# Kernel optimization log

Hardware: AMD Instinct MI355X
Metric: run time of the kernel (lower is better)

The kernel has to match this reference:

```python
import jax, jax.numpy as jnp
import numpy as np

N_WIRES = 4
N_LAYERS = 2
DIM = 2 ** N_WIRES  # 16
EPS = 1e-5

# PennyLane convention: wire 0 is the most-significant bit of the basis index.
def _bit(i, w):
    return (i >> (N_WIRES - 1 - w)) & 1

# CNOT(control=w, target=(w+1)%N_WIRES) as a basis-state permutation on [DIM]
def _cnot_perm(c, t):
    perm = np.arange(DIM)
    for i in range(DIM):
        if _bit(i, c) == 1:
            perm[i] = i ^ (1 << (N_WIRES - 1 - t))
    return jnp.asarray(perm)

CNOT_PERMS = [_cnot_perm(w, (w + 1) % N_WIRES) for w in range(N_WIRES)]

# PauliZ expectation signs: +1 if bit w of basis state is 0 else -1, shape [N_WIRES, DIM]
SIGNS = jnp.asarray(np.array([[1.0 - 2.0 * _bit(i, w) for i in range(DIM)]
                              for w in range(N_WIRES)], dtype=np.float32))

def _rx(t):
    c = jnp.cos(t / 2).astype(jnp.complex64)
    s = (-1j * jnp.sin(t / 2)).astype(jnp.complex64)
    return jnp.stack([jnp.stack([c, s], -1), jnp.stack([s, c], -1)], -2)

def _ry(t):
    c = jnp.cos(t / 2).astype(jnp.complex64)
    s = jnp.sin(t / 2).astype(jnp.complex64)
    return jnp.stack([jnp.stack([c, -s], -1), jnp.stack([s, c], -1)], -2)

def _rz(t):
    e0 = jnp.exp(-1j * t.astype(jnp.complex64) / 2)
    e1 = jnp.exp(1j * t.astype(jnp.complex64) / 2)
    z = jnp.zeros_like(e0)
    return jnp.stack([jnp.stack([e0, z], -1), jnp.stack([z, e1], -1)], -2)

def _apply1q(state, U, w):
    # state: [B, DIM] complex64; U: [2,2] (shared) or [B,2,2] (per-sample)
    B = state.shape[0]
    st = state.reshape(B, 2 ** w, 2, 2 ** (N_WIRES - 1 - w))
    if U.ndim == 3:
        st = jnp.einsum('blkr,bjk->bljr', st, U)
    else:
        st = jnp.einsum('blkr,jk->bljr', st, U)
    return st.reshape(B, DIM)

def _circuit(angles, weights):
    # angles: [B, N_WIRES] float32, weights: [N_LAYERS, N_WIRES, 3]
    B = angles.shape[0]
    state = jnp.zeros((B, DIM), jnp.complex64).at[:, 0].set(1.0)
    # AngleEmbedding: RX(angle) per wire (per-sample angles)
    for w in range(N_WIRES):
        state = _apply1q(state, _rx(angles[:, w]), w)
    for l in range(N_LAYERS):
        for w in range(N_WIRES):
            state = _apply1q(state, _rx(weights[l, w, 0]), w)
            state = _apply1q(state, _ry(weights[l, w, 1]), w)
            state = _apply1q(state, _rz(weights[l, w, 2]), w)
        for w in range(N_WIRES):
            state = state[:, CNOT_PERMS[w]]
    probs = state.real ** 2 + state.imag ** 2  # [B, DIM]
    return probs @ SIGNS.T  # [B, N_WIRES]

def setup_inputs() -> dict:
    key = jax.random.key(0)
    k1, k2 = jax.random.split(key)
    B = 131072
    x = jax.random.normal(k1, (B, 1, 12, 12), dtype=jnp.float32)
    weights = jax.random.normal(k2, (N_LAYERS, N_WIRES, 3), dtype=jnp.float32)
    gamma = jnp.ones((N_WIRES,), jnp.float32)
    beta = jnp.zeros((N_WIRES,), jnp.float32)
    return {"x": x, "weights": weights, "gamma": gamma, "beta": beta}

def reference(x, weights, gamma, beta):
    B = x.shape[0]
    # avg_pool2d(kernel=6, stride=6) on [B,1,12,12] -> [B,1,2,2] -> [B,4]
    pooled = x.reshape(B, 1, 2, 6, 2, 6).mean(axis=(3, 5)).reshape(B, N_WIRES)
    q = _circuit(pooled, weights)  # [B, 4]
    # dropout p=0 is identity; BatchNorm1d (training mode: batch stats, biased var)
    mean = q.mean(axis=0)
    var = q.var(axis=0)
    return (q - mean) / jnp.sqrt(var + EPS) * gamma + beta
```

## Files before the change

### kernel.cpp

```cpp
#include <hip/hip_runtime.h>

#define WS_SUMS   352
#define N_REP     8

__global__ void k_pre(const float* __restrict__ W, float* __restrict__ ws){
  __shared__ float Ur[16][16];
  __shared__ float Uim[16][16];
  __shared__ float Mr[4][16][16];
  __shared__ float Mi[4][16][16];
  const int t = threadIdx.x;

  if (t < N_REP*8) ws[WS_SUMS + t] = 0.f;

  if (t < 16){
    float re[16], im[16];
    #pragma unroll
    for (int i = 0; i < 16; i++){ re[i] = 0.f; im[i] = 0.f; }
    re[t] = 1.f;

    #pragma unroll
    for (int l = 0; l < 2; l++){
      #pragma unroll
      for (int w = 0; w < 4; w++){
        const int m = 8 >> w;
        const float* g = W + (l*4 + w)*3;
        {
          float th = 0.5f*g[0], c = cosf(th), s = sinf(th);
          #pragma unroll
          for (int i0 = 0; i0 < 16; i0++) if (!(i0 & m)){
            int i1 = i0 | m;
            float a0r=re[i0], a0i=im[i0], a1r=re[i1], a1i=im[i1];
            re[i0] = c*a0r + s*a1i;  im[i0] = c*a0i - s*a1r;
            re[i1] = c*a1r + s*a0i;  im[i1] = c*a1i - s*a0r;
          }
        }
        {
          float th = 0.5f*g[1], c = cosf(th), s = sinf(th);
          #pragma unroll
          for (int i0 = 0; i0 < 16; i0++) if (!(i0 & m)){
            int i1 = i0 | m;
            float a0r=re[i0], a0i=im[i0], a1r=re[i1], a1i=im[i1];
            re[i0] = c*a0r - s*a1r;  im[i0] = c*a0i - s*a1i;
            re[i1] = s*a0r + c*a1r;  im[i1] = s*a0i + c*a1i;
          }
        }
        {
          float th = 0.5f*g[2], c = cosf(th), s = sinf(th);
          #pragma unroll
          for (int i0 = 0; i0 < 16; i0++) if (!(i0 & m)){
            int i1 = i0 | m;
            float a0r=re[i0], a0i=im[i0], a1r=re[i1], a1i=im[i1];
            re[i0] = c*a0r + s*a0i;  im[i0] = c*a0i - s*a0r;
            re[i1] = c*a1r - s*a1i;  im[i1] = c*a1i + s*a1r;
          }
        }
      }
      #pragma unroll
      for (int w = 0; w < 4; w++){
        const int mc = 8 >> w, mt = 8 >> ((w+1)&3);
        float nr[16], ni[16];
        #pragma unroll
        for (int i = 0; i < 16; i++){
          int src = (i & mc) ? (i ^ mt) : i;
          nr[i] = re[src]; ni[i] = im[src];
        }
        #pragma unroll
        for (int i = 0; i < 16; i++){ re[i] = nr[i]; im[i] = ni[i]; }
      }
    }
    #pragma unroll
    for (int k = 0; k < 16; k++){ Ur[k][t] = re[k]; Uim[k][t] = im[k]; }
  }
  __syncthreads();

  {
    const int j = t >> 4, i = t & 15;
    #pragma unroll
    for (int w = 0; w < 4; w++){
      const int zm = 8 >> w;
      float mr = 0.f, mi = 0.f;
      #pragma unroll
      for (int k = 0; k < 16; k++){
        float z = (k & zm) ? -1.f : 1.f;
        float ar = Ur[k][j], ai = Uim[k][j];
        float br = Ur[k][i], bi = Uim[k][i];
        mr += z*(ar*br + ai*bi);
        mi += z*(ar*bi - ai*br);
      }
      Mr[w][j][i] = mr;  Mi[w][j][i] = mi;
    }
  }
  __syncthreads();

  if (t < 81){
    int d0 = t/27, rem = t - d0*27;
    int d1 = rem/9;  rem -= d1*9;
    int d2 = rem/3,  d3 = rem - d2*3;
    int maskY = 0, maskZ = 0, mY = 0;
    if (d0 == 1){ maskY |= 8; mY++; } else if (d0 == 2) maskZ |= 8;
    if (d1 == 1){ maskY |= 4; mY++; } else if (d1 == 2) maskZ |= 4;
    if (d2 == 1){ maskY |= 2; mY++; } else if (d2 == 2) maskZ |= 2;
    if (d3 == 1){ maskY |= 1; mY++; } else if (d3 == 2) maskZ |= 1;
    const int mall = maskY | maskZ;
    const int sel  = mY & 3;
    #pragma unroll
    for (int w = 0; w < 4; w++){
      float c = 0.f;
      for (int i = 0; i < 16; i++){
        int j = i ^ maskY;
        float s = (__popc(i & mall) & 1) ? -1.f : 1.f;
        float val = (sel == 0) ?  Mr[w][j][i]
                  : (sel == 1) ?  Mi[w][j][i]
                  : (sel == 2) ? -Mr[w][j][i]
                  :              -Mi[w][j][i];
        c += s * val;
      }
      ws[t*4 + w] = c * 0.0625f;
    }
  }
}

__global__ __launch_bounds__(256) void k_main(const float* __restrict__ x,
                                              const float* __restrict__ C,
                                              float* __restrict__ qout,
                                              float* __restrict__ sums){
  __shared__ float wred[4][8];
  const int t = threadIdx.x;
  const size_t row = (size_t)blockIdx.x*256 + t;
  const float4* rp = (const float4*)(x + row*144);

  float aTL = 0.f, aTR = 0.f, aBL = 0.f, aBR = 0.f;
  #pragma unroll
  for (int ph = 0; ph < 3; ph++){
    float4 buf[12];
    #pragma unroll
    for (int j = 0; j < 12; j++) buf[j] = rp[ph*12 + j];
    #pragma unroll
    for (int j = 0; j < 12; j++){
      const int p  = ph*12 + j;
      const int cg = p % 3;
      float s01 = buf[j].x + buf[j].y, s23 = buf[j].z + buf[j].w;
      float L = (cg == 0) ? (s01 + s23) : ((cg == 1) ? s01 : 0.f);
      float R = (cg == 2) ? (s01 + s23) : ((cg == 1) ? s23 : 0.f);
      if (p < 18){ aTL += L; aTR += R; } else { aBL += L; aBR += R; }
    }
  }

  const float inv = 1.f/36.f;
  float s0,c0,s1,c1,s2,c2,s3,c3;
  __sincosf(aTL*inv, &s0, &c0);
  __sincosf(aTR*inv, &s1, &c1);
  __sincosf(aBL*inv, &s2, &c2);
  __sincosf(aBR*inv, &s3, &c3);
  const float g0[3] = {1.f, -s0, c0};
  const float g1[3] = {1.f, -s1, c1};
  const float g2[3] = {1.f, -s2, c2};
  const float g3[3] = {1.f, -s3, c3};

  float G01[9], G23[9];
  #pragma unroll
  for (int a = 0; a < 3; a++)
    #pragma unroll
    for (int b = 0; b < 3; b++){
      G01[a*3+b] = g0[a]*g1[b];
      G23[a*3+b] = g2[a]*g3[b];
    }

  float q0=0.f, q1=0.f, q2=0.f, q3=0.f;
  #pragma unroll
  for (int m = 0; m < 9; m++){
    #pragma unroll
    for (int l = 0; l < 9; l++){
      const int n = m*9 + l;
      float g = G01[m]*G23[l];
      q0 = fmaf(C[n*4+0], g, q0);
      q1 = fmaf(C[n*4+1], g, q1);
      q2 = fmaf(C[n*4+2], g, q2);
      q3 = fmaf(C[n*4+3], g, q3);
    }
  }

  ((float4*)qout)[row] = make_float4(q0, q1, q2, q3);

  float red[8] = {q0, q1, q2, q3, q0*q0, q1*q1, q2*q2, q3*q3};
  #pragma unroll
  for (int off = 32; off >= 1; off >>= 1){
    #pragma unroll
    for (int k = 0; k < 8; k++) red[k] += __shfl_down(red[k], off, 64);
  }
  const int lane = t & 63, wv = t >> 6;
  if (lane == 0){
    #pragma unroll
    for (int k = 0; k < 8; k++) wred[wv][k] = red[k];
  }
  __syncthreads();
  if (t < 8){
    float s = wred[0][t] + wred[1][t] + wred[2][t] + wred[3][t];
    atomicAdd(&sums[(blockIdx.x & (N_REP-1))*8 + t], s);
  }
}

__global__ __launch_bounds__(256) void k_statsnorm(float* __restrict__ out,
                                                   const float* __restrict__ sums,
                                                   const float* __restrict__ gamma,
                                                   const float* __restrict__ beta,
                                                   float invB){
  const int idx = blockIdx.x*256 + threadIdx.x;
  float sc[4], sh[4];
  #pragma unroll
  for (int w = 0; w < 4; w++){
    float s1 = 0.f, s2 = 0.f;
    #pragma unroll
    for (int rep = 0; rep < N_REP; rep++){
      s1 += sums[rep*8 + w];
      s2 += sums[rep*8 + 4 + w];
    }
    float mean  = s1 * invB;
    float var   = s2 * invB - mean*mean;
    float scale = gamma[w] * rsqrtf(var + 1e-5f);
    sc[w] = scale;
    sh[w] = fmaf(-mean, scale, beta[w]);
  }
  float4* o4 = (float4*)out;
  float4 qv = o4[idx];
  qv.x = fmaf(qv.x, sc[0], sh[0]);
  qv.y = fmaf(qv.y, sc[1], sh[1]);
  qv.z = fmaf(qv.z, sc[2], sh[2]);
  qv.w = fmaf(qv.w, sc[3], sh[3]);
  o4[idx] = qv;
}

extern "C" void kernel_launch(void* const* d_in, const int* in_sizes, int n_in,
                              void* d_out, int out_size, void* d_ws, size_t ws_size,
                              hipStream_t stream){
  const float* x     = (const float*)d_in[0];
  const float* W     = (const float*)d_in[1];
  const float* gamma = (const float*)d_in[2];
  const float* beta  = (const float*)d_in[3];
  float* ws  = (float*)d_ws;
  float* out = (float*)d_out;
  const int B = in_sizes[0] / 144;

  k_pre<<<1, 256, 0, stream>>>(W, ws);
  k_main<<<B/256, 256, 0, stream>>>(x, ws, out, ws + WS_SUMS);
  k_statsnorm<<<B/256, 256, 0, stream>>>(out, ws + WS_SUMS, gamma, beta, 1.f/(float)B);
}
```

Measured before the change: 145.2 us.

## Split each row across four threads with coalesced loads and shuffle reductions

k_main now assigns four threads per sample row. Each thread loads 9 interleaved float4s, so a quad reads contiguous memory instead of each thread streaming its own 576-byte row, and pooled partial sums are combined with xor shuffles. Each thread then computes one of the four expectation outputs, so the 81-term contraction is split four ways and the output is written as a coalesced scalar store. The grid grows fourfold, and the per-lane reduction tree is shortened in exchange for a few redundant sincos calls per quad. A pragma unroll is also added to a loop in the precompute kernel.

New measurement: 143.5 us. Within noise of the previous version (-1.2%).

```diff
diff --git a/kernel.cpp b/kernel.cpp
--- a/kernel.cpp
+++ b/kernel.cpp
@@ -106,6 +106,7 @@
     #pragma unroll
     for (int w = 0; w < 4; w++){
       float c = 0.f;
+      #pragma unroll
       for (int i = 0; i < 16; i++){
         int j = i ^ maskY;
         float s = (__popc(i & mall) & 1) ? -1.f : 1.f;
@@ -126,24 +127,31 @@
                                               float* __restrict__ sums){
   __shared__ float wred[4][8];
   const int t = threadIdx.x;
-  const size_t row = (size_t)blockIdx.x*256 + t;
-  const float4* rp = (const float4*)(x + row*144);
+  const int k = t & 3;
+  const size_t row = (size_t)blockIdx.x*64 + (t >> 2);
+  const float4* rp4 = (const float4*)(x) + row*36;
+
+  float4 v[9];
+  #pragma unroll
+  for (int j = 0; j < 9; j++) v[j] = rp4[j*4 + k];
 
   float aTL = 0.f, aTR = 0.f, aBL = 0.f, aBR = 0.f;
   #pragma unroll
-  for (int ph = 0; ph < 3; ph++){
-    float4 buf[12];
-    #pragma unroll
-    for (int j = 0; j < 12; j++) buf[j] = rp[ph*12 + j];
-    #pragma unroll
-    for (int j = 0; j < 12; j++){
-      const int p  = ph*12 + j;
-      const int cg = p % 3;
-      float s01 = buf[j].x + buf[j].y, s23 = buf[j].z + buf[j].w;
-      float L = (cg == 0) ? (s01 + s23) : ((cg == 1) ? s01 : 0.f);
-      float R = (cg == 2) ? (s01 + s23) : ((cg == 1) ? s23 : 0.f);
-      if (p < 18){ aTL += L; aTR += R; } else { aBL += L; aBR += R; }
-    }
+  for (int j = 0; j < 9; j++){
+    const int p  = j*4 + k;
+    const int cg = p % 3;
+    float s01 = v[j].x + v[j].y, s23 = v[j].z + v[j].w;
+    float L = (cg == 0) ? (s01 + s23) : ((cg == 1) ? s01 : 0.f);
+    float R = (cg == 2) ? (s01 + s23) : ((cg == 1) ? s23 : 0.f);
+    if (p < 18){ aTL += L; aTR += R; } else { aBL += L; aBR += R; }
+  }
+
+  #pragma unroll
+  for (int m = 1; m <= 2; m <<= 1){
+    aTL += __shfl_xor(aTL, m, 64);
+    aTR += __shfl_xor(aTR, m, 64);
+    aBL += __shfl_xor(aBL, m, 64);
+    aBR += __shfl_xor(aBR, m, 64);
   }
 
   const float inv = 1.f/36.f;
@@ -166,33 +174,26 @@
       G23[a*3+b] = g2[a]*g3[b];
     }
 
-  float q0=0.f, q1=0.f, q2=0.f, q3=0.f;
+  float q = 0.f;
   #pragma unroll
   for (int m = 0; m < 9; m++){
     #pragma unroll
     for (int l = 0; l < 9; l++){
       const int n = m*9 + l;
-      float g = G01[m]*G23[l];
-      q0 = fmaf(C[n*4+0], g, q0);
-      q1 = fmaf(C[n*4+1], g, q1);
-      q2 = fmaf(C[n*4+2], g, q2);
-      q3 = fmaf(C[n*4+3], g, q3);
-    }
-  }
-
-  ((float4*)qout)[row] = make_float4(q0, q1, q2, q3);
-
-  float red[8] = {q0, q1, q2, q3, q0*q0, q1*q1, q2*q2, q3*q3};
-  #pragma unroll
-  for (int off = 32; off >= 1; off >>= 1){
-    #pragma unroll
-    for (int k = 0; k < 8; k++) red[k] += __shfl_down(red[k], off, 64);
+      q = fmaf(C[n*4 + k], G01[m]*G23[l], q);
+    }
+  }
+
+  qout[(size_t)blockIdx.x*256 + t] = q;
+
+  float qs = q, q2 = q*q;
+  #pragma unroll
+  for (int off = 32; off >= 4; off >>= 1){
+    qs += __shfl_down(qs, off, 64);
+    q2 += __shfl_down(q2, off, 64);
   }
   const int lane = t & 63, wv = t >> 6;
-  if (lane == 0){
-    #pragma unroll
-    for (int k = 0; k < 8; k++) wred[wv][k] = red[k];
-  }
+  if (lane < 4){ wred[wv][lane] = qs; wred[wv][lane+4] = q2; }
   __syncthreads();
   if (t < 8){
     float s = wred[0][t] + wred[1][t] + wred[2][t] + wred[3][t];
@@ -242,6 +243,6 @@
   const int B = in_sizes[0] / 144;
 
   k_pre<<<1, 256, 0, stream>>>(W, ws);
-  k_main<<<B/256, 256, 0, stream>>>(x, ws, out, ws + WS_SUMS);
+  k_main<<<B/64, 256, 0, stream>>>(x, ws, out, ws + WS_SUMS);
   k_statsnorm<<<B/256, 256, 0, stream>>>(out, ws + WS_SUMS, gamma, beta, 1.f/(float)B);
 }
```
